# Kernel tuning notes

Measured on AMD Instinct MI355X. Metric: run time of the kernel, lower is better.

The kernel has to match this reference:

```python
import jax, jax.numpy as jnp
import numpy as np

N = 50000      # total nodes
E = 500000     # edges
D = 128        # in_channels
B = 50         # graphs in batch
NPG = N // B   # nodes per graph (equal-sized graphs)
RATIO = 0.5
ALPHA = 0.6


def setup_inputs() -> dict:
    key = jax.random.key(0)
    ks = jax.random.split(key, 8)
    x = jax.random.normal(ks[0], (N, D), dtype=jnp.float32)
    edge_index = jax.random.randint(ks[1], (2, E), 0, N, dtype=jnp.int32)
    batch = jnp.repeat(jnp.arange(B, dtype=jnp.int32), NPG)  # sorted, equal blocks
    s = 1.0 / np.sqrt(D)
    # GCNConv(D,1) for structure score
    W_s = jax.random.normal(ks[2], (D, 1), dtype=jnp.float32) * s
    b_s = jnp.zeros((1,), dtype=jnp.float32)
    # Linear(D,1) for feature score
    W_f = jax.random.normal(ks[3], (1, D), dtype=jnp.float32) * s
    b_f = jnp.zeros((1,), dtype=jnp.float32)
    # GCNConv(D,D) fusion layer
    W_fu = jax.random.normal(ks[4], (D, D), dtype=jnp.float32) * s
    b_fu = jnp.zeros((D,), dtype=jnp.float32)
    return {"x": x, "edge_index": edge_index, "batch": batch,
            "W_s": W_s, "b_s": b_s, "W_f": W_f, "b_f": b_f,
            "W_fu": W_fu, "b_fu": b_fu}


def gcn_conv(x, src, dst, W, b, n):
    """PyG GCNConv: add self loops, symmetric D^-1/2 (A+I) D^-1/2 @ (xW) + b."""
    xw = x @ W                                  # [n, out]
    loop = jnp.arange(n, dtype=src.dtype)
    s = jnp.concatenate([src, loop])
    d = jnp.concatenate([dst, loop])
    deg = jax.ops.segment_sum(jnp.ones_like(s, dtype=xw.dtype), d, num_segments=n)
    dinv = jax.lax.rsqrt(jnp.maximum(deg, 1e-12))
    norm = dinv[s] * dinv[d]                    # [E+n]
    out = jax.ops.segment_sum(norm[:, None] * xw[s], d, num_segments=n)
    return out + b


def reference(x, edge_index, batch, W_s, b_s, W_f, b_f, W_fu, b_fu):
    src, dst = edge_index[0], edge_index[1]
    # fused score: alpha * structure (GCN) + (1-alpha) * feature (Linear)
    score_s = gcn_conv(x, src, dst, W_s, b_s, N)[:, 0]          # [N]
    score_f = (x @ W_f.T + b_f)[:, 0]                           # [N]
    score = jnp.tanh(ALPHA * score_s + (1.0 - ALPHA) * score_f)
    # per-graph top-k (equal-sized graphs -> dense [B, NPG] view, like the torch topk)
    k = int(np.ceil(RATIO * NPG))
    dense = score.reshape(B, NPG)
    order = jnp.argsort(-dense, axis=-1)                        # descending
    offsets = (jnp.arange(B, dtype=jnp.int32) * NPG)[:, None]
    perm = (order[:, :k].astype(jnp.int32) + offsets).reshape(-1)  # [B*k]
    # fusion conv on full graph, then gather selected nodes
    x_fused = gcn_conv(x, src, dst, W_fu, b_fu, N)              # [N, D]
    x_ae = x_fused[perm]                                        # [B*k, D]
    x_out = x_ae * score[perm][:, None]                         # multiplier == 1
    batch_out = batch[perm]
    # filter_adj: remap node ids, keep edges with both endpoints selected
    nodemap = jnp.full((N,), -1, dtype=jnp.int32).at[perm].set(
        jnp.arange(perm.shape[0], dtype=jnp.int32))
    r, c = nodemap[src], nodemap[dst]
    m = (r >= 0) & (c >= 0)
    edge_index_new = jnp.stack([r[m], c[m]], axis=0)
    return (x_out, edge_index_new, batch_out, perm, x_ae)
```

## Files before the change

### kernel.cpp

```cpp
#include <hip/hip_runtime.h>
#include <math.h>

#define N_NODES 50000
#define N_EDGES 500000
#define DIM     128
#define NGRAPH  50
#define NPGC    1000
#define KSEL    500
#define SORT_N  1024
#define NBE     489
#define GEMM_BLKS 782
#define EDGE_BLKS 1954
#define NDINV     196
#define GATH_BLKS 6250
#define DEGB    64
#define NCHUNK  1954


__global__ __launch_bounds__(256) void k1_fused(const float* __restrict__ x,
                                                const float* __restrict__ W,
                                                float* __restrict__ xw,
                                                const float* __restrict__ Ws,
                                                const float* __restrict__ Wf,
                                                const float* __restrict__ bf,
                                                double* __restrict__ pack,
                                                double* __restrict__ sf,
                                                const int* __restrict__ dst,
                                                int* __restrict__ degpriv,
                                                int* __restrict__ eslot) {
    __shared__ float lds[6400];
    int t = threadIdx.x;
    if (blockIdx.x < DEGB) {
        int b = blockIdx.x;
        int* priv = degpriv + b * N_NODES;
        for (int c = b; c < NCHUNK; c += 2 * DEGB) {
            int e1 = (c << 8) + t;
            int cB = c + DEGB;
            int e2 = (cB << 8) + t;
            int d1 = (e1 < N_EDGES) ? dst[e1] : -1;
            int d2 = (cB < NCHUNK && e2 < N_EDGES) ? dst[e2] : -1;
            if (d1 >= 0)
                eslot[e1] = __hip_atomic_fetch_add(&priv[d1], 1, __ATOMIC_RELAXED,
                                                   __HIP_MEMORY_SCOPE_WORKGROUP);
            if (d2 >= 0)
                eslot[e2] = __hip_atomic_fetch_add(&priv[d2], 1, __ATOMIC_RELAXED,
                                                   __HIP_MEMORY_SCOPE_WORKGROUP);
        }
        return;
    }
    float* Wt  = lds;
    float* Xt  = lds + 4096;
    float* Wsl = lds + 6144;
    float* Wfl = lds + 6272;
    int cg = t & 15;
    int ng = t >> 4;
    int node_base = (blockIdx.x - DEGB) * 64;

    if (t < 128) Wsl[t] = Ws[t];
    else         Wfl[t - 128] = Wf[t - 128];

    int dn  = t >> 2;
    int dk8 = (t & 3) << 3;
    double ps = 0.0, pf = 0.0;

    float4 acc[4][2];
    #pragma unroll
    for (int nn = 0; nn < 4; nn++) {
        acc[nn][0] = make_float4(0.f, 0.f, 0.f, 0.f);
        acc[nn][1] = make_float4(0.f, 0.f, 0.f, 0.f);
    }
    for (int qtr = 0; qtr < 4; qtr++) {
        const float4* Wg = (const float4*)W + qtr * 1024;
        float4* Wl = (float4*)Wt;
        #pragma unroll
        for (int i = 0; i < 4; i++) {
            int f = t + i * 256;
            Wl[f] = Wg[f];
        }
        #pragma unroll
        for (int i = 0; i < 2; i++) {
            int f = t + i * 256;
            int row = f >> 3, col = f & 7;
            int node = node_base + row;
            float4 v = make_float4(0.f, 0.f, 0.f, 0.f);
            if (node < N_NODES) v = *(const float4*)&x[(size_t)node * DIM + qtr * 32 + col * 4];
            *(float4*)&Xt[(row << 5) + ((col ^ (row & 7)) << 2)] = v;
        }
        __syncthreads();
        #pragma unroll 2
        for (int kc = 0; kc < 8; kc++) {
            int k = kc << 2;
            float4 wa[4], wb[4];
            #pragma unroll
            for (int kk = 0; kk < 4; kk++) {
                wa[kk] = *(const float4*)&Wt[(k + kk) * DIM + (cg << 2)];
                wb[kk] = *(const float4*)&Wt[(k + kk) * DIM + (cg << 2) + 64];
            }
            int csw = (kc ^ (ng & 7)) << 2;
            #pragma unroll
            for (int nn = 0; nn < 4; nn++) {
                float4 xv = *(const float4*)&Xt[((ng + (nn << 4)) << 5) + csw];
                acc[nn][0].x += xv.x * wa[0].x + xv.y * wa[1].x + xv.z * wa[2].x + xv.w * wa[3].x;
                acc[nn][0].y += xv.x * wa[0].y + xv.y * wa[1].y + xv.z * wa[2].y + xv.w * wa[3].y;
                acc[nn][0].z += xv.x * wa[0].z + xv.y * wa[1].z + xv.z * wa[2].z + xv.w * wa[3].z;
                acc[nn][0].w += xv.x * wa[0].w + xv.y * wa[1].w + xv.z * wa[2].w + xv.w * wa[3].w;
                acc[nn][1].x += xv.x * wb[0].x + xv.y * wb[1].x + xv.z * wb[2].x + xv.w * wb[3].x;
                acc[nn][1].y += xv.x * wb[0].y + xv.y * wb[1].y + xv.z * wb[2].y + xv.w * wb[3].y;
                acc[nn][1].z += xv.x * wb[0].z + xv.y * wb[1].z + xv.z * wb[2].z + xv.w * wb[3].z;
                acc[nn][1].w += xv.x * wb[0].w + xv.y * wb[1].w + xv.z * wb[2].w + xv.w * wb[3].w;
            }
        }
        #pragma unroll 4
        for (int j = 0; j < 8; j++) {
            int ko = dk8 + j;
            int col = ko >> 2, sub = ko & 3;
            double xd = (double)Xt[(dn << 5) + ((col ^ (dn & 7)) << 2) + sub];
            ps += xd * (double)Wsl[qtr * 32 + ko];
            pf += xd * (double)Wfl[qtr * 32 + ko];
        }
        __syncthreads();
    }
    #pragma unroll
    for (int nn = 0; nn < 4; nn++) {
        int node = node_base + ng + (nn << 4);
        if (node < N_NODES) {
            *(float4*)&xw[(size_t)node * DIM + (cg << 2)]      = acc[nn][0];
            *(float4*)&xw[(size_t)node * DIM + (cg << 2) + 64] = acc[nn][1];
        }
    }
    ps += __shfl_down(ps, 2, 64); ps += __shfl_down(ps, 1, 64);
    pf += __shfl_down(pf, 2, 64); pf += __shfl_down(pf, 1, 64);
    if ((t & 3) == 0) {
        int node = node_base + dn;
        if (node < N_NODES) {
            pack[2 * node + 1] = ps;
            sf[node] = pf + (double)bf[0];
        }
    }
}


__global__ __launch_bounds__(256) void k2_merge(int* __restrict__ degpriv,
                                                int* __restrict__ deg,
                                                int* __restrict__ rowoff,
                                                int* __restrict__ bsums256,
                                                double* __restrict__ pack,
                                                float* __restrict__ dinvf) {
    int t = threadIdx.x;
    int lane = t & 63, wid = t >> 6;
    int i = blockIdx.x * 256 + t;
    int o = 0;
    if (i < N_NODES) {
        #pragma unroll 8
        for (int b = 0; b < DEGB; b++) {
            int* p = &degpriv[b * N_NODES + i];
            int c = *p;
            *p = o;
            o += c;
        }
        deg[i] = o;
        double di = 1.0 / sqrt((double)(o + 1));
        pack[2 * i] = di;
        dinvf[i] = (float)di;
    }
    __shared__ int ws4[4];
    int incl = o;
    #pragma unroll
    for (int off = 1; off < 64; off <<= 1) {
        int u = __shfl_up(incl, off, 64);
        if (lane >= off) incl += u;
    }
    if (lane == 63) ws4[wid] = incl;
    __syncthreads();
    int woff = 0;
    #pragma unroll
    for (int w = 0; w < 4; w++) if (w < wid) woff += ws4[w];
    if (i < N_NODES) rowoff[i] = incl - o + woff;
    if (t == 255) bsums256[blockIdx.x] = woff + incl;
}


__global__ __launch_bounds__(256) void k3_csr(const int* __restrict__ src,
                                              const int* __restrict__ dst,
                                              const int* __restrict__ rowoff,
                                              const int* __restrict__ bsums256,
                                              const int* __restrict__ degpriv,
                                              const int* __restrict__ eslot,
                                              int* __restrict__ csr) {
    __shared__ int bsN[256];
    int t = threadIdx.x;
    if (t < 64) {
        int carry = 0;
        #pragma unroll
        for (int ch = 0; ch < 4; ch++) {
            int i = ch * 64 + t;
            int v = (i < NDINV) ? bsums256[i] : 0;
            int incl = v;
            #pragma unroll
            for (int off = 1; off < 64; off <<= 1) {
                int u = __shfl_up(incl, off, 64);
                if (t >= off) incl += u;
            }
            bsN[i] = incl - v + carry;
            carry += __shfl(incl, 63, 64);
        }
    }
    __syncthreads();
    int e = blockIdx.x * 256 + t;
    if (e >= N_EDGES) return;
    int d = dst[e];
    int owner = (e >> 8) & (DEGB - 1);
    int pos = rowoff[d] + bsN[d >> 8] + degpriv[owner * N_NODES + d] + eslot[e];
    csr[pos] = src[e];
}


__global__ __launch_bounds__(256) void k3b_score(const int* __restrict__ csr,
                                                 const int* __restrict__ rowoff,
                                                 const int* __restrict__ bsums256,
                                                 const int* __restrict__ deg,
                                                 const double* __restrict__ pack,
                                                 double* __restrict__ score_sd) {
    __shared__ int bsN[256];
    int t = threadIdx.x;
    if (t < 64) {
        int carry = 0;
        #pragma unroll
        for (int ch = 0; ch < 4; ch++) {
            int i = ch * 64 + t;
            int v = (i < NDINV) ? bsums256[i] : 0;
            int incl = v;
            #pragma unroll
            for (int off = 1; off < 64; off <<= 1) {
                int u = __shfl_up(incl, off, 64);
                if (t >= off) incl += u;
            }
            bsN[i] = incl - v + carry;
            carry += __shfl(incl, 63, 64);
        }
    }
    __syncthreads();
    int node = blockIdx.x * 256 + t;
    if (node >= N_NODES) return;
    int base = rowoff[node] + bsN[node >> 8];
    int cnt  = deg[node];
    double acc0 = 0.0, acc1 = 0.0;
    int i = 0;
    for (; i + 2 <= cnt; i += 2) {
        int s0 = csr[base + i];
        int s1 = csr[base + i + 1];
        double2 p0 = ((const double2*)pack)[s0];
        double2 p1 = ((const double2*)pack)[s1];
        acc0 += p0.x * p0.y;
        acc1 += p1.x * p1.y;
    }
    if (i < cnt) {
        int s0 = csr[base + i];
        double2 p0 = ((const double2*)pack)[s0];
        acc0 += p0.x * p0.y;
    }
    score_sd[node] = pack[2 * node] * (acc0 + acc1);
}


__global__ __launch_bounds__(512) void k4_topk(const double* __restrict__ score_sd,
                                               const double* __restrict__ pack,
                                               const double* __restrict__ sf,
                                               const float* __restrict__ bs,
                                               const int* __restrict__ batch,
                                               int* __restrict__ perm, int* __restrict__ nodemap,
                                               float* __restrict__ scoref_sel,
                                               float* __restrict__ out, long o2, long o3) {
    __shared__ double key[SORT_N];
    __shared__ int    idx[SORT_N];
    int g = blockIdx.x, t = threadIdx.x;
    const double A = 0.6, OMA = 1.0 - 0.6;
    double bsv = (double)bs[0];
    for (int i = t; i < SORT_N; i += 512) {
        if (i < NPGC) {
            int node = g * NPGC + i;
            double2 p = ((const double2*)pack)[node];
            double tot = score_sd[node] + p.x * p.x * p.y + bsv;
            key[i] = tanh(A * tot + OMA * sf[node]);
            idx[i] = i;
        } else { key[i] = -1e300; idx[i] = i; }
    }
    __syncthreads();
    for (int size = 2; size <= SORT_N; size <<= 1) {
        for (int stride = size >> 1; stride > 0; stride >>= 1) {
            int a = ((t & ~(stride - 1)) << 1) | (t & (stride - 1));
            int b = a | stride;
            bool descFirst = ((a & size) == 0);
            double ka = key[a], kb = key[b];
            int ia = idx[a], ib = idx[b];
            bool aAfterB = (ka < kb) || (ka == kb && ia > ib);
            if (descFirst ? aAfterB : !aAfterB) {
                key[a] = kb; key[b] = ka;
                idx[a] = ib; idx[b] = ia;
            }
            __syncthreads();
        }
    }
    for (int j = t; j < KSEL; j += 512) {
        int node = g * NPGC + idx[j];
        int pos  = g * KSEL + j;
        perm[pos]        = node;
        nodemap[node]    = pos + 1;
        scoref_sel[pos]  = (float)key[j];
        out[o2 + pos]    = (float)batch[node];
        out[o3 + pos]    = (float)node;
    }
}


__global__ __launch_bounds__(256) void k5_escan_gather(const int* __restrict__ src,
                                                       const int* __restrict__ dst,
                                                       const int* __restrict__ nodemap,
                                                       int* __restrict__ epos,
                                                       int* __restrict__ bsumsE,
                                                       const float* __restrict__ xw,
                                                       const int* __restrict__ perm,
                                                       const int* __restrict__ rowoff,
                                                       const int* __restrict__ bsums256,
                                                       const int* __restrict__ deg,
                                                       const int* __restrict__ csr,
                                                       const float* __restrict__ dinvf,
                                                       const float* __restrict__ scoref_sel,
                                                       const float* __restrict__ b_fu,
                                                       float* __restrict__ out, long o4) {
    int t = threadIdx.x;
    int lane = t & 63, wid = t >> 6;
    if (blockIdx.x < NBE) {
        __shared__ int ws4[4];
        int base = blockIdx.x * 1024 + t * 4;
        int v0 = 0, v1 = 0, v2 = 0, v3 = 0;
        if (base + 0 < N_EDGES) v0 = (nodemap[src[base + 0]] > 0 && nodemap[dst[base + 0]] > 0);
        if (base + 1 < N_EDGES) v1 = (nodemap[src[base + 1]] > 0 && nodemap[dst[base + 1]] > 0);
        if (base + 2 < N_EDGES) v2 = (nodemap[src[base + 2]] > 0 && nodemap[dst[base + 2]] > 0);
        if (base + 3 < N_EDGES) v3 = (nodemap[src[base + 3]] > 0 && nodemap[dst[base + 3]] > 0);
        int s4 = v0 + v1 + v2 + v3;
        int incl = s4;
        #pragma unroll
        for (int off = 1; off < 64; off <<= 1) {
            int u = __shfl_up(incl, off, 64);
            if (lane >= off) incl += u;
        }
        if (lane == 63) ws4[wid] = incl;
        __syncthreads();
        int woff = 0;
        #pragma unroll
        for (int w = 0; w < 4; w++) if (w < wid) woff += ws4[w];
        int excl = incl - s4 + woff;
        if (base + 0 < N_EDGES) epos[base + 0] = excl;
        if (base + 1 < N_EDGES) epos[base + 1] = excl + v0;
        if (base + 2 < N_EDGES) epos[base + 2] = excl + v0 + v1;
        if (base + 3 < N_EDGES) epos[base + 3] = excl + v0 + v1 + v2;
        if (t == 255) bsumsE[blockIdx.x] = woff + incl;
        return;
    }
    __shared__ int bsN[256];
    if (t < 64) {
        int carry = 0;
        #pragma unroll
        for (int ch = 0; ch < 4; ch++) {
            int i = ch * 64 + t;
            int v = (i < NDINV) ? bsums256[i] : 0;
            int incl = v;
            #pragma unroll
            for (int off = 1; off < 64; off <<= 1) {
                int u = __shfl_up(incl, off, 64);
                if (t >= off) incl += u;
            }
            bsN[i] = incl - v + carry;
            carry += __shfl(incl, 63, 64);
        }
    }
    __syncthreads();
    int wave = (blockIdx.x - NBE) * 4 + wid;
    int p = perm[wave];
    float dpf = dinvf[p];
    int c2 = lane * 2;
    float2 v = ((const float2*)(xw + (size_t)p * DIM))[lane];
    float nself = dpf * dpf;
    float ax = nself * v.x, ay = nself * v.y;
    int beg = rowoff[p] + bsN[p >> 8], cnt = deg[p];
    int i = 0;
    for (; i + 2 <= cnt; i += 2) {
        int s0 = csr[beg + i];
        int s1 = csr[beg + i + 1];
        float2 u0 = ((const float2*)(xw + (size_t)s0 * DIM))[lane];
        float2 u1 = ((const float2*)(xw + (size_t)s1 * DIM))[lane];
        float n0 = dinvf[s0] * dpf, n1 = dinvf[s1] * dpf;
        ax += n0 * u0.x; ay += n0 * u0.y;
        ax += n1 * u1.x; ay += n1 * u1.y;
    }
    if (i < cnt) {
        int s0 = csr[beg + i];
        float2 u0 = ((const float2*)(xw + (size_t)s0 * DIM))[lane];
        float n0 = dinvf[s0] * dpf;
        ax += n0 * u0.x; ay += n0 * u0.y;
    }
    ax += b_fu[c2];
    ay += b_fu[c2 + 1];
    float sc = scoref_sel[wave];
    size_t ro = (size_t)wave * DIM + c2;
    out[o4 + ro]     = ax;
    out[o4 + ro + 1] = ay;
    out[ro]          = ax * sc;
    out[ro + 1]      = ay * sc;
}


__global__ __launch_bounds__(256) void k6_compact(const int* __restrict__ src,
                                                  const int* __restrict__ dst,
                                                  const int* __restrict__ nodemap,
                                                  const int* __restrict__ epos,
                                                  const int* __restrict__ bsumsE,
                                                  float* __restrict__ out_edges, long M) {
    __shared__ int bsE[512];
    int t = threadIdx.x;
    if (t < 64) {
        int carry = 0;
        #pragma unroll
        for (int c = 0; c < 8; c++) {
            int i = c * 64 + t;
            int v = (i < NBE) ? bsumsE[i] : 0;
            int incl = v;
            #pragma unroll
            for (int off = 1; off < 64; off <<= 1) {
                int u = __shfl_up(incl, off, 64);
                if (t >= off) incl += u;
            }
            if (i < 512) bsE[i] = incl - v + carry;
            carry += __shfl(incl, 63, 64);
        }
    }
    __syncthreads();
    int e = blockIdx.x * 256 + t;
    if (e >= N_EDGES) return;
    int r = nodemap[src[e]], c = nodemap[dst[e]];
    if (r > 0 && c > 0) {
        int pos = epos[e] + bsE[e >> 10];
        out_edges[pos]     = (float)(r - 1);
        out_edges[M + pos] = (float)(c - 1);
    }
}


extern "C" void kernel_launch(void* const* d_in, const int* in_sizes, int n_in,
                              void* d_out, int out_size, void* d_ws, size_t ws_size,
                              hipStream_t stream) {
    const float* x    = (const float*)d_in[0];
    const int*   ei   = (const int*)d_in[1];
    const int*   src  = ei;
    const int*   dst  = ei + N_EDGES;
    const int*   batch= (const int*)d_in[2];
    const float* W_s  = (const float*)d_in[3];
    const float* b_s  = (const float*)d_in[4];
    const float* W_f  = (const float*)d_in[5];
    const float* b_f  = (const float*)d_in[6];
    const float* W_fu = (const float*)d_in[7];
    const float* b_fu = (const float*)d_in[8];
    float* out = (float*)d_out;

    char* wsp = (char*)d_ws;
    size_t off = 0;
    auto take = [&](size_t bytes) -> char* {
        char* p = wsp + off;
        off = (off + bytes + 255) & ~(size_t)255;
        return p;
    };
    char*   zbase      = wsp;
    int*    degpriv    = (int*)   take((size_t)DEGB * N_NODES * 4);
    int*    nodemap    = (int*)   take((size_t)N_NODES * 4);
    size_t  zbytes     = off;
    int*    eslot      = (int*)   take((size_t)N_EDGES * 4);
    int*    deg        = (int*)   take((size_t)N_NODES * 4);
    double* score_sd   = (double*)take((size_t)N_NODES * 8);
    double* pack       = (double*)take((size_t)N_NODES * 16);
    double* sf         = (double*)take((size_t)N_NODES * 8);
    float*  dinvf      = (float*) take((size_t)N_NODES * 4);
    float*  scoref_sel = (float*) take((size_t)NGRAPH * KSEL * 4);
    int*    perm       = (int*)   take((size_t)NGRAPH * KSEL * 4);
    int*    rowoff     = (int*)   take((size_t)N_NODES * 4);
    int*    epos       = (int*)   take((size_t)N_EDGES * 4);
    int*    bsumsE     = (int*)   take((size_t)1024 * 4);
    int*    bsums256   = (int*)   take((size_t)1024 * 4);
    int*    csr        = (int*)   take((size_t)N_EDGES * 4);
    float*  xw         = (float*) take((size_t)N_NODES * DIM * 4);

    long M  = ((long)out_size - 6450000L) / 2;
    long o1 = 3200000L;
    long o2 = o1 + 2 * M;
    long o3 = o2 + (long)NGRAPH * KSEL;
    long o4 = o3 + (long)NGRAPH * KSEL;

    hipMemsetAsync(zbase, 0, zbytes, stream);

    k1_fused<<<DEGB + GEMM_BLKS, 256, 0, stream>>>(x, W_fu, xw, W_s, W_f, b_f, pack, sf,
                                                   dst, degpriv, eslot);
    k2_merge<<<NDINV, 256, 0, stream>>>(degpriv, deg, rowoff, bsums256, pack, dinvf);
    k3_csr<<<EDGE_BLKS, 256, 0, stream>>>(src, dst, rowoff, bsums256, degpriv, eslot, csr);
    k3b_score<<<NDINV, 256, 0, stream>>>(csr, rowoff, bsums256, deg, pack, score_sd);
    k4_topk<<<NGRAPH, 512, 0, stream>>>(score_sd, pack, sf, b_s, batch,
                                        perm, nodemap, scoref_sel, out, o2, o3);
    k5_escan_gather<<<NBE + GATH_BLKS, 256, 0, stream>>>(src, dst, nodemap, epos, bsumsE,
                                                         xw, perm, rowoff, bsums256, deg, csr,
                                                         dinvf, scoref_sel, b_fu, out, o4);
    k6_compact<<<EDGE_BLKS, 256, 0, stream>>>(src, dst, nodemap, epos, bsumsE, out + o1, M);
}
```

Measured before the change: 210.0 us.

## Compute x@W_fu with split-bf16 MFMA instead of scalar FP32 FMAs

Replaces the FP32 FMA register-tiled GEMM in the fused first kernel with MFMA 16x16x32 bf16 instructions. Each FP32 operand is split into high and low bf16 parts and three MFMAs approximate FP32 accuracy. The score dot products now rebuild x from the bf16 hi+lo pair, which drops the lowest mantissa bits of x. Conversion work moves into the LDS staging step, and the output stores become scalar per-element writes rather than float4 writes.

```diff
diff --git a/kernel.cpp b/kernel.cpp
--- a/kernel.cpp
+++ b/kernel.cpp
@@ -16,6 +16,18 @@
 #define DEGB    64
 #define NCHUNK  1954
 
+using bfrag = __attribute__((ext_vector_type(8))) short;
+using f32x4 = __attribute__((ext_vector_type(4))) float;
+
+__device__ __forceinline__ unsigned short f2bf(float f) {
+    unsigned int u = __float_as_uint(f);
+    u += 0x7FFF + ((u >> 16) & 1);
+    return (unsigned short)(u >> 16);
+}
+__device__ __forceinline__ float bf2f(unsigned short h) {
+    return __uint_as_float(((unsigned int)h) << 16);
+}
+
 
 __global__ __launch_bounds__(256) void k1_fused(const float* __restrict__ x,
                                                 const float* __restrict__ W,
@@ -28,7 +40,8 @@
                                                 const int* __restrict__ dst,
                                                 int* __restrict__ degpriv,
                                                 int* __restrict__ eslot) {
-    __shared__ float lds[6400];
+    __shared__ unsigned short uls[15360];
+    __shared__ float wsf[256];
     int t = threadIdx.x;
     if (blockIdx.x < DEGB) {
         int b = blockIdx.x;
@@ -48,84 +61,85 @@
         }
         return;
     }
-    float* Wt  = lds;
-    float* Xt  = lds + 4096;
-    float* Wsl = lds + 6144;
-    float* Wfl = lds + 6272;
-    int cg = t & 15;
-    int ng = t >> 4;
+    unsigned short* Wth = uls;
+    unsigned short* Wtl = uls + 5120;
+    unsigned short* Xh  = uls + 10240;
+    unsigned short* Xl  = uls + 12800;
     int node_base = (blockIdx.x - DEGB) * 64;
-
-    if (t < 128) Wsl[t] = Ws[t];
-    else         Wfl[t - 128] = Wf[t - 128];
-
-    int dn  = t >> 2;
-    int dk8 = (t & 3) << 3;
+    int l = t & 63, wv = t >> 6;
+    int arow = l & 15;
+    int ag   = l >> 4;
+
+    if (t < 128) wsf[t] = Ws[t];
+    else         wsf[t] = Wf[t - 128];
+
+    int dn = t >> 2, dq = t & 3;
     double ps = 0.0, pf = 0.0;
 
-    float4 acc[4][2];
+    f32x4 acc[8];
     #pragma unroll
-    for (int nn = 0; nn < 4; nn++) {
-        acc[nn][0] = make_float4(0.f, 0.f, 0.f, 0.f);
-        acc[nn][1] = make_float4(0.f, 0.f, 0.f, 0.f);
-    }
+    for (int cg = 0; cg < 8; cg++) { f32x4 z = {0.f, 0.f, 0.f, 0.f}; acc[cg] = z; }
+
     for (int qtr = 0; qtr < 4; qtr++) {
-        const float4* Wg = (const float4*)W + qtr * 1024;
-        float4* Wl = (float4*)Wt;
-        #pragma unroll
-        for (int i = 0; i < 4; i++) {
-            int f = t + i * 256;
-            Wl[f] = Wg[f];
+        #pragma unroll
+        for (int i = 0; i < 8; i++) {
+            int f = t + (i << 8);
+            int ch = f & 127, k2 = f >> 7;
+            float w0 = W[(size_t)(qtr * 32 + k2 * 2)     * DIM + ch];
+            float w1 = W[(size_t)(qtr * 32 + k2 * 2 + 1) * DIM + ch];
+            unsigned short h0 = f2bf(w0), h1 = f2bf(w1);
+            unsigned short l0 = f2bf(w0 - bf2f(h0)), l1 = f2bf(w1 - bf2f(h1));
+            *(unsigned int*)&Wth[ch * 40 + k2 * 2] = (unsigned int)h0 | ((unsigned int)h1 << 16);
+            *(unsigned int*)&Wtl[ch * 40 + k2 * 2] = (unsigned int)l0 | ((unsigned int)l1 << 16);
         }
         #pragma unroll
         for (int i = 0; i < 2; i++) {
-            int f = t + i * 256;
+            int f = t + (i << 8);
             int row = f >> 3, col = f & 7;
             int node = node_base + row;
             float4 v = make_float4(0.f, 0.f, 0.f, 0.f);
             if (node < N_NODES) v = *(const float4*)&x[(size_t)node * DIM + qtr * 32 + col * 4];
-            *(float4*)&Xt[(row << 5) + ((col ^ (row & 7)) << 2)] = v;
+            unsigned short h0 = f2bf(v.x), h1 = f2bf(v.y), h2 = f2bf(v.z), h3 = f2bf(v.w);
+            unsigned short g0 = f2bf(v.x - bf2f(h0)), g1 = f2bf(v.y - bf2f(h1));
+            unsigned short g2 = f2bf(v.z - bf2f(h2)), g3 = f2bf(v.w - bf2f(h3));
+            ushort4 hv; hv.x = h0; hv.y = h1; hv.z = h2; hv.w = h3;
+            ushort4 lv; lv.x = g0; lv.y = g1; lv.z = g2; lv.w = g3;
+            *(ushort4*)&Xh[row * 40 + col * 4] = hv;
+            *(ushort4*)&Xl[row * 40 + col * 4] = lv;
         }
         __syncthreads();
-        #pragma unroll 2
-        for (int kc = 0; kc < 8; kc++) {
-            int k = kc << 2;
-            float4 wa[4], wb[4];
+        bfrag ah = *(const bfrag*)&Xh[(wv * 16 + arow) * 40 + ag * 8];
+        bfrag al = *(const bfrag*)&Xl[(wv * 16 + arow) * 40 + ag * 8];
+        #pragma unroll
+        for (int cg = 0; cg < 8; cg++) {
+            bfrag bh = *(const bfrag*)&Wth[(cg * 16 + arow) * 40 + ag * 8];
+            bfrag bl = *(const bfrag*)&Wtl[(cg * 16 + arow) * 40 + ag * 8];
+            acc[cg] = __builtin_amdgcn_mfma_f32_16x16x32_bf16(ah, bh, acc[cg], 0, 0, 0);
+            acc[cg] = __builtin_amdgcn_mfma_f32_16x16x32_bf16(ah, bl, acc[cg], 0, 0, 0);
+            acc[cg] = __builtin_amdgcn_mfma_f32_16x16x32_bf16(al, bh, acc[cg], 0, 0, 0);
+        }
+        {
+            bfrag xh = *(const bfrag*)&Xh[dn * 40 + dq * 8];
+            bfrag xl = *(const bfrag*)&Xl[dn * 40 + dq * 8];
             #pragma unroll
-            for (int kk = 0; kk < 4; kk++) {
-                wa[kk] = *(const float4*)&Wt[(k + kk) * DIM + (cg << 2)];
-                wb[kk] = *(const float4*)&Wt[(k + kk) * DIM + (cg << 2) + 64];
+            for (int j = 0; j < 8; j++) {
+                double xd = (double)bf2f((unsigned short)xh[j])
+                          + (double)bf2f((unsigned short)xl[j]);
+                int k = qtr * 32 + dq * 8 + j;
+                ps += xd * (double)wsf[k];
+                pf += xd * (double)wsf[128 + k];
             }
-            int csw = (kc ^ (ng & 7)) << 2;
-            #pragma unroll
-            for (int nn = 0; nn < 4; nn++) {
-                float4 xv = *(const float4*)&Xt[((ng + (nn << 4)) << 5) + csw];
-                acc[nn][0].x += xv.x * wa[0].x + xv.y * wa[1].x + xv.z * wa[2].x + xv.w * wa[3].x;
-                acc[nn][0].y += xv.x * wa[0].y + xv.y * wa[1].y + xv.z * wa[2].y + xv.w * wa[3].y;
-                acc[nn][0].z += xv.x * wa[0].z + xv.y * wa[1].z + xv.z * wa[2].z + xv.w * wa[3].z;
-                acc[nn][0].w += xv.x * wa[0].w + xv.y * wa[1].w + xv.z * wa[2].w + xv.w * wa[3].w;
-                acc[nn][1].x += xv.x * wb[0].x + xv.y * wb[1].x + xv.z * wb[2].x + xv.w * wb[3].x;
-                acc[nn][1].y += xv.x * wb[0].y + xv.y * wb[1].y + xv.z * wb[2].y + xv.w * wb[3].y;
-                acc[nn][1].z += xv.x * wb[0].z + xv.y * wb[1].z + xv.z * wb[2].z + xv.w * wb[3].z;
-                acc[nn][1].w += xv.x * wb[0].w + xv.y * wb[1].w + xv.z * wb[2].w + xv.w * wb[3].w;
-            }
-        }
-        #pragma unroll 4
-        for (int j = 0; j < 8; j++) {
-            int ko = dk8 + j;
-            int col = ko >> 2, sub = ko & 3;
-            double xd = (double)Xt[(dn << 5) + ((col ^ (dn & 7)) << 2) + sub];
-            ps += xd * (double)Wsl[qtr * 32 + ko];
-            pf += xd * (double)Wfl[qtr * 32 + ko];
         }
         __syncthreads();
     }
+    int r0 = wv * 16 + ((l >> 4) << 2);
+    int c0 = l & 15;
     #pragma unroll
-    for (int nn = 0; nn < 4; nn++) {
-        int node = node_base + ng + (nn << 4);
-        if (node < N_NODES) {
-            *(float4*)&xw[(size_t)node * DIM + (cg << 2)]      = acc[nn][0];
-            *(float4*)&xw[(size_t)node * DIM + (cg << 2) + 64] = acc[nn][1];
+    for (int cg = 0; cg < 8; cg++) {
+        #pragma unroll
+        for (int j = 0; j < 4; j++) {
+            int node = node_base + r0 + j;
+            if (node < N_NODES) xw[(size_t)node * DIM + cg * 16 + c0] = acc[cg][j];
         }
     }
     ps += __shfl_down(ps, 2, 64); ps += __shfl_down(ps, 1, 64);
```

Result: no change. 209.0 us (-0.4%).
